# Kernel tuning notes

Hardware: AMD Instinct MI355X
Metric: run time of the kernel (lower is better)

## Reference

```python
import math
import jax, jax.numpy as jnp
import numpy as np

B, S_IN, S_OUT, D_IN, D_OUT = 8, 4096, 1024, 128, 128
EPS = 1e-5


def setup_inputs() -> dict:
    key = jax.random.key(0)
    k0, k1, k2, k3 = jax.random.split(key, 4)
    x = jax.random.normal(k0, (B, S_IN, D_IN), dtype=jnp.float32)
    M = jax.random.uniform(k1, (D_OUT, D_IN), minval=-0.5, maxval=0.5, dtype=jnp.float32)
    P = jax.random.uniform(k2, (D_OUT, D_OUT), minval=-0.1, maxval=0.1, dtype=jnp.float32)
    Linker = jax.random.uniform(k3, (S_IN, S_OUT), minval=-0.1, maxval=0.1, dtype=jnp.float32)
    gamma = jnp.ones((D_OUT,), dtype=jnp.float32)   # LayerNorm weight
    beta = jnp.zeros((D_OUT,), dtype=jnp.float32)   # LayerNorm bias
    return {"x": x, "M": M, "P": P, "Linker": Linker, "gamma": gamma, "beta": beta}


def reference(x, M, P, Linker, gamma, beta):
    # x: (B, S, in_dim) -> out: (B, S_out, out_dim)
    Bsz, S, _ = x.shape
    D = M.shape[0]
    x_trans = x @ M.T                                   # (B, S, D)
    mu = jnp.mean(x_trans, axis=-1, keepdims=True)
    var = jnp.var(x_trans, axis=-1, keepdims=True)      # biased, matches torch LayerNorm
    x_trans = (x_trans - mu) / jnp.sqrt(var + EPS) * gamma + beta
    # periods[i, j] = i*D + j + 2 (registered buffer)
    idx = jnp.arange(D)
    periods = (idx[:, None] * D + idx[None, :] + 2).astype(jnp.float32)  # (D, D)
    k = jnp.arange(S, dtype=jnp.float32)[:, None, None]                   # (S, 1, 1)
    phi = jnp.cos(2.0 * math.pi * k / periods)                            # (S, D, D)
    M_k = P[None, :, :] * phi                                             # (S, D, D)
    Nk = jnp.einsum('bsj,sij->bsi', x_trans, M_k)                         # (B, S, D)
    out = jnp.einsum('bsi,st->bti', Nk, Linker)                           # (B, S_out, D)
    return out
```

## Files before the change

kernel.cpp:

```cpp
#include <hip/hip_runtime.h>
#include <math.h>

#define B_SZ   8
#define S_INN  4096
#define S_OUTT 1024
#define DD     128
#define EPS_LN 1e-5f

typedef _Float16 h2 __attribute__((ext_vector_type(2)));
typedef _Float16 h4 __attribute__((ext_vector_type(4)));
typedef _Float16 h8 __attribute__((ext_vector_type(8)));
typedef float f32x4 __attribute__((ext_vector_type(4)));

#define XN_OFF   0
#define NT_OFF   6291456
#define LT_OFF   8388608

__device__ __forceinline__ void gload16(const void* g, void* l) {
    __builtin_amdgcn_global_load_lds(
        (const __attribute__((address_space(1))) unsigned int*)g,
        (__attribute__((address_space(3))) unsigned int*)l, 16, 0, 0);
}

__device__ __forceinline__ float fdot2_(h2 a, h2 b, float c) {
#if __has_builtin(__builtin_amdgcn_fdot2)
    return __builtin_amdgcn_fdot2(a, b, c, false);
#else
    return fmaf((float)a[0], (float)b[0], fmaf((float)a[1], (float)b[1], c));
#endif
}

__device__ __forceinline__ float fract_(float x) {
#if __has_builtin(__builtin_amdgcn_fractf)
    return __builtin_amdgcn_fractf(x);
#else
    return x - floorf(x);
#endif
}

__global__ __launch_bounds__(256) void kA(const float* __restrict__ x,
                                          const float* __restrict__ M,
                                          const float* __restrict__ gamma,
                                          const float* __restrict__ beta,
                                          _Float16* __restrict__ xn16) {
    __shared__ float Ms[128 * 128];

    const int tid = threadIdx.x;
    #pragma unroll
    for (int k = 0; k < 16; ++k) {
        int e4 = tid + k * 256;
        int i  = e4 >> 5;
        int j4 = e4 & 31;
        float4 v = *(const float4*)&M[i * DD + j4 * 4];
        int igp = (i >> 4) & 7;
        int qp  = (i >> 2) & 3;
        int cp  = i & 3;
        int col = (qp * 8 + igp) * 4 + cp;
        Ms[(j4 * 4 + 0) * 128 + col] = v.x;
        Ms[(j4 * 4 + 1) * 128 + col] = v.y;
        Ms[(j4 * 4 + 2) * 128 + col] = v.z;
        Ms[(j4 * 4 + 3) * 128 + col] = v.w;
    }
    __syncthreads();

    const int ig = tid & 7;
    const int rg = tid >> 3;
    const int row0 = blockIdx.x * 64 + rg * 2;

    float acc[2][16];
    #pragma unroll
    for (int rr = 0; rr < 2; ++rr)
        #pragma unroll
        for (int k = 0; k < 16; ++k) acc[rr][k] = 0.f;

    const float4* xr[2];
    #pragma unroll
    for (int rr = 0; rr < 2; ++rr) xr[rr] = (const float4*)&x[(size_t)(row0 + rr) * DD];

    for (int j4 = 0; j4 < 32; ++j4) {
        float xvf[2][4];
        #pragma unroll
        for (int rr = 0; rr < 2; ++rr) {
            float4 t = xr[rr][j4];
            xvf[rr][0] = t.x; xvf[rr][1] = t.y; xvf[rr][2] = t.z; xvf[rr][3] = t.w;
        }
        #pragma unroll
        for (int c = 0; c < 4; ++c) {
            const float* Mrow = &Ms[(j4 * 4 + c) * 128];
            #pragma unroll
            for (int q = 0; q < 4; ++q) {
                const float4 mv = *(const float4*)&Mrow[(q * 8 + ig) * 4];
                #pragma unroll
                for (int rr = 0; rr < 2; ++rr) {
                    acc[rr][q * 4 + 0] = fmaf(xvf[rr][c], mv.x, acc[rr][q * 4 + 0]);
                    acc[rr][q * 4 + 1] = fmaf(xvf[rr][c], mv.y, acc[rr][q * 4 + 1]);
                    acc[rr][q * 4 + 2] = fmaf(xvf[rr][c], mv.z, acc[rr][q * 4 + 2]);
                    acc[rr][q * 4 + 3] = fmaf(xvf[rr][c], mv.w, acc[rr][q * 4 + 3]);
                }
            }
        }
    }

    float g[16], be[16];
    #pragma unroll
    for (int q = 0; q < 4; ++q) {
        float4 gv = *(const float4*)&gamma[ig * 16 + q * 4];
        float4 bv = *(const float4*)&beta[ig * 16 + q * 4];
        g[q*4+0]=gv.x; g[q*4+1]=gv.y; g[q*4+2]=gv.z; g[q*4+3]=gv.w;
        be[q*4+0]=bv.x; be[q*4+1]=bv.y; be[q*4+2]=bv.z; be[q*4+3]=bv.w;
    }
    #pragma unroll
    for (int rr = 0; rr < 2; ++rr) {
        float s1 = 0.f, s2 = 0.f;
        #pragma unroll
        for (int k = 0; k < 16; ++k) { s1 += acc[rr][k]; s2 = fmaf(acc[rr][k], acc[rr][k], s2); }
        #pragma unroll
        for (int m = 1; m < 8; m <<= 1) {
            s1 += __shfl_xor(s1, m, 64);
            s2 += __shfl_xor(s2, m, 64);
        }
        float mu  = s1 * (1.f / 128.f);
        float var = s2 * (1.f / 128.f) - mu * mu;
        float rstd = rsqrtf(var + EPS_LN);
        _Float16* dst = &xn16[(size_t)(row0 + rr) * DD + ig * 16];
        #pragma unroll
        for (int q = 0; q < 4; ++q) {
            h4 hv;
            hv[0] = (_Float16)((acc[rr][q*4+0] - mu) * rstd * g[q*4+0] + be[q*4+0]);
            hv[1] = (_Float16)((acc[rr][q*4+1] - mu) * rstd * g[q*4+1] + be[q*4+1]);
            hv[2] = (_Float16)((acc[rr][q*4+2] - mu) * rstd * g[q*4+2] + be[q*4+2]);
            hv[3] = (_Float16)((acc[rr][q*4+3] - mu) * rstd * g[q*4+3] + be[q*4+3]);
            *(h4*)&dst[q * 4] = hv;
        }
    }
}

__global__ __launch_bounds__(256) void kB(const _Float16* __restrict__ xn16,
                                          const float* __restrict__ P,
                                          _Float16* __restrict__ NT) {
    const int s0 = blockIdx.x * 8;
    __shared__ _Float16 Ps[128 * 136];
    __shared__ _Float16 xs[8 * 1024];

    const int tid = threadIdx.x;
    #pragma unroll
    for (int k = 0; k < 4; ++k) {
        int c   = tid + k * 256;
        int row = c >> 4;
        int b   = row >> 3, sl = row & 7;
        int kk  = c & 15;
        h8 v = *(const h8*)&xn16[((size_t)b * S_INN + s0 + sl) * DD + kk * 8];
        #pragma unroll
        for (int q = 0; q < 4; ++q) {
            int j2 = kk * 4 + q;
            int slot = (j2 & 15) * 4 + (j2 >> 4);
            *(h2*)&xs[sl * 1024 + slot * 16 + b * 2] = h2{ v[q * 2], v[q * 2 + 1] };
        }
    }
    #pragma unroll
    for (int k = 0; k < 16; ++k) {
        int e4 = tid + k * 256;
        int ip = e4 >> 5, j4 = e4 & 31;
        float4 v = *(const float4*)&P[ip * DD + j4 * 4];
        *(h4*)&Ps[ip * 136 + j4 * 4] = h4{ (_Float16)v.x, (_Float16)v.y,
                                           (_Float16)v.z, (_Float16)v.w };
    }
    __syncthreads();

    const int il = tid >> 2;
    const int jq = tid & 3;
    const int j0base = jq * 32;
    const float s0f = (float)s0;
    const float pb0 = (float)(il * DD + j0base + 2);
    const int bsel = ((jq & 1) << 2) | (jq & 2);

    float invp0[32], invp1[32];
    #pragma unroll
    for (int jj = 0; jj < 32; ++jj) {
        float pf0 = pb0 + (float)jj;
        invp0[jj] = __builtin_amdgcn_rcpf(pf0);
        invp1[jj] = __builtin_amdgcn_rcpf(pf0 + 8192.f);
    }

    h8 st[4];
    #pragma unroll
    for (int s_ = 0; s_ < 4; ++s_) st[s_] = h8{};

    #pragma unroll
    for (int sl = 0; sl < 8; ++sl) {
        const float sf = s0f + (float)sl;
        float acc0[8] = {0,0,0,0,0,0,0,0};
        float acc1[8] = {0,0,0,0,0,0,0,0};

        #pragma unroll
        for (int j8 = 0; j8 < 4; ++j8) {
            h8 p0 = *(const h8*)&Ps[il * 136 + j0base + j8 * 8];
            h8 p1 = *(const h8*)&Ps[(il + 64) * 136 + j0base + j8 * 8];

            h2 w0[4], w1[4];
            #pragma unroll
            for (int cp = 0; cp < 4; ++cp) {
                float wv0[2], wv1[2];
                #pragma unroll
                for (int u = 0; u < 2; ++u) {
                    int c = cp * 2 + u;
                    int jj = j8 * 8 + c;
                    float r0 = fract_(sf * invp0[jj]);
                    wv0[u] = (float)p0[c] * __builtin_amdgcn_cosf(r0);
                    float r1 = fract_(sf * invp1[jj]);
                    wv1[u] = (float)p1[c] * __builtin_amdgcn_cosf(r1);
                }
                w0[cp] = h2{ (_Float16)wv0[0], (_Float16)wv0[1] };
                w1[cp] = h2{ (_Float16)wv1[0], (_Float16)wv1[1] };
            }

            #pragma unroll
            for (int jp = 0; jp < 4; ++jp) {
                int slot = (j8 * 4 + jp) * 4 + jq;
                const h8 xlo = *(const h8*)&xs[sl * 1024 + slot * 16];
                const h8 xhi = *(const h8*)&xs[sl * 1024 + slot * 16 + 8];
                #pragma unroll
                for (int b = 0; b < 4; ++b) {
                    h2 xa = h2{ xlo[b * 2], xlo[b * 2 + 1] };
                    h2 xb = h2{ xhi[b * 2], xhi[b * 2 + 1] };
                    acc0[b]     = fdot2_(w0[jp], xa, acc0[b]);
                    acc0[b + 4] = fdot2_(w0[jp], xb, acc0[b + 4]);
                    acc1[b]     = fdot2_(w1[jp], xa, acc1[b]);
                    acc1[b + 4] = fdot2_(w1[jp], xb, acc1[b + 4]);
                }
            }
        }

        const bool lo1 = (jq & 1) == 0;
        const bool lo2 = (jq & 2) == 0;
        float n0[4], n1[4];
        #pragma unroll
        for (int k = 0; k < 4; ++k) {
            float mine   = lo1 ? acc0[k] : acc0[k + 4];
            float theirs = lo1 ? acc0[k + 4] : acc0[k];
            n0[k] = mine + __shfl_xor(theirs, 1, 64);
            float mine1   = lo1 ? acc1[k] : acc1[k + 4];
            float theirs1 = lo1 ? acc1[k + 4] : acc1[k];
            n1[k] = mine1 + __shfl_xor(theirs1, 1, 64);
        }
        #pragma unroll
        for (int k = 0; k < 2; ++k) {
            float mine   = lo2 ? n0[k] : n0[k + 2];
            float theirs = lo2 ? n0[k + 2] : n0[k];
            float r0 = mine + __shfl_xor(theirs, 2, 64);
            float mine1   = lo2 ? n1[k] : n1[k + 2];
            float theirs1 = lo2 ? n1[k + 2] : n1[k];
            float r1 = mine1 + __shfl_xor(theirs1, 2, 64);
            st[k][sl]     = (_Float16)r0;
            st[2 + k][sl] = (_Float16)r1;
        }
    }

    #pragma unroll
    for (int k = 0; k < 2; ++k) {
        *(h8*)&NT[((size_t)(bsel + k) * DD + il) * S_INN + s0]        = st[k];
        *(h8*)&NT[((size_t)(bsel + k) * DD + il + 64) * S_INN + s0]   = st[2 + k];
    }
}

__global__ __launch_bounds__(256) void kXf(const float* __restrict__ src,
                                           _Float16* __restrict__ dst,
                                           int R, int C) {
    const size_t sb = (size_t)blockIdx.z * (size_t)R * C;
    const int r0 = blockIdx.x * 64, c0 = blockIdx.y * 64;
    __shared__ float tile[64][67];
    const int tid = threadIdx.x;
    {
        const int lr = tid >> 2, lc = (tid & 3) * 16;
        const float4* srow = (const float4*)&src[sb + (size_t)(r0 + lr) * C + c0 + lc];
        float4 v0 = srow[0], v1 = srow[1], v2 = srow[2], v3 = srow[3];
        *(float4*)&tile[lr][lc +  0] = v0;
        *(float4*)&tile[lr][lc +  4] = v1;
        *(float4*)&tile[lr][lc +  8] = v2;
        *(float4*)&tile[lr][lc + 12] = v3;
    }
    __syncthreads();
    {
        const int wc = tid >> 2, wsx = (tid & 3) * 16;
        h8 o0, o1;
        #pragma unroll
        for (int k = 0; k < 8; ++k) o0[k] = (_Float16)tile[wsx + k][wc];
        #pragma unroll
        for (int k = 0; k < 8; ++k) o1[k] = (_Float16)tile[wsx + 8 + k][wc];
        _Float16* drow = &dst[sb + (size_t)(c0 + wc) * R + r0 + wsx];
        *(h8*)&drow[0] = o0;
        *(h8*)&drow[8] = o1;
    }
}

__global__ __launch_bounds__(512) void kC(const _Float16* __restrict__ NT,
                                          const _Float16* __restrict__ LT,
                                          float* __restrict__ part) {
    __shared__ _Float16 lds_pool[4 * 8192];

    const int tid  = threadIdx.x;
    const int lane = tid & 63;
    const int w    = tid >> 6;
    const int wm   = w >> 2;
    const int wn   = w & 3;
    const int lr   = lane & 15;
    const int lh   = lane >> 4;

    const int mt = blockIdx.x >> 3;
    const int nt = blockIdx.x & 7;
    const int kz = blockIdx.y;
    const int t0 = mt * 128;
    const int n0 = nt * 128;
    const int sbase = kz * 1024;

    const int swz = (lr & 7) << 4;

    f32x4 acc[4][2];
    #pragma unroll
    for (int m = 0; m < 4; ++m)
        #pragma unroll
        for (int n = 0; n < 2; ++n) acc[m][n] = (f32x4){0.f, 0.f, 0.f, 0.f};

    auto stage = [&](int buf, int s0) {
        _Float16* base = &lds_pool[buf * 16384];
        #pragma unroll
        for (int ro = 0; ro < 2; ++ro) {
            int idx = tid + ro * 512;
            int r   = idx >> 3;
            int kb  = idx & 7;
            int skb = kb ^ (r & 7);
            gload16(&LT[(size_t)(t0 + r) * S_INN + s0 + skb * 8], base + idx * 8);
            gload16(&NT[(size_t)(n0 + r) * S_INN + s0 + skb * 8], base + 8192 + idx * 8);
        }
    };

    auto compute = [&](int buf) {
        const char* ldsA = (const char*)&lds_pool[buf * 16384];
        const char* ldsB = ldsA + 16384;
        #pragma unroll
        for (int kk = 0; kk < 2; ++kk) {
            const int kb = (kk * 64 + lh * 16) ^ swz;
            h8 a[4], bf[2];
            #pragma unroll
            for (int m = 0; m < 4; ++m)
                a[m] = *(const h8*)(ldsA + (wm * 64 + m * 16 + lr) * 128 + kb);
            #pragma unroll
            for (int n = 0; n < 2; ++n)
                bf[n] = *(const h8*)(ldsB + (wn * 32 + n * 16 + lr) * 128 + kb);
            #pragma unroll
            for (int m = 0; m < 4; ++m)
                #pragma unroll
                for (int n = 0; n < 2; ++n)
                    acc[m][n] = __builtin_amdgcn_mfma_f32_16x16x32_f16(a[m], bf[n], acc[m][n], 0, 0, 0);
        }
    };

    stage(0, sbase);
    __syncthreads();
    for (int st = 0; st < 16; ++st) {
        const int cur = st & 1;
        if (st < 15) stage(cur ^ 1, sbase + (st + 1) * 64);
        compute(cur);
        __syncthreads();
    }

    float* dst = &part[(size_t)(kz * B_SZ + nt) * S_OUTT * DD];
    #pragma unroll
    for (int m = 0; m < 4; ++m) {
        const int t = t0 + wm * 64 + m * 16 + lh * 4;
        #pragma unroll
        for (int n = 0; n < 2; ++n) {
            const int i = wn * 32 + n * 16 + lr;
            #pragma unroll
            for (int r = 0; r < 4; ++r)
                dst[(size_t)(t + r) * DD + i] = acc[m][n][r];
        }
    }
}

__global__ __launch_bounds__(256) void kD(const float* __restrict__ part,
                                          float* __restrict__ out) {
    const int e4 = blockIdx.x * 256 + threadIdx.x;
    const float4* p = (const float4*)part;
    float4 a  = p[e4];
    float4 b1 = p[e4 + 262144];
    float4 c1 = p[e4 + 2 * 262144];
    float4 d1 = p[e4 + 3 * 262144];
    float4 o;
    o.x = a.x + b1.x + c1.x + d1.x;
    o.y = a.y + b1.y + c1.y + d1.y;
    o.z = a.z + b1.z + c1.z + d1.z;
    o.w = a.w + b1.w + c1.w + d1.w;
    ((float4*)out)[e4] = o;
}

extern "C" void kernel_launch(void* const* d_in, const int* in_sizes, int n_in,
                              void* d_out, int out_size, void* d_ws, size_t ws_size,
                              hipStream_t stream) {
    const float* x     = (const float*)d_in[0];
    const float* M     = (const float*)d_in[1];
    const float* P     = (const float*)d_in[2];
    const float* Lk    = (const float*)d_in[3];
    const float* gamma = (const float*)d_in[4];
    const float* beta  = (const float*)d_in[5];
    float* out = (float*)d_out;

    float* wsf = (float*)d_ws;
    _Float16*  xn16 = (_Float16*)(wsf + XN_OFF);
    _Float16*  NT   = (_Float16*)(wsf + NT_OFF);
    _Float16*  LT   = (_Float16*)(wsf + LT_OFF);
    float*     part = wsf + XN_OFF;

    hipLaunchKernelGGL(kA,  dim3(512),        dim3(256), 0, stream, x, M, gamma, beta, xn16);
    hipLaunchKernelGGL(kB,  dim3(512),        dim3(256), 0, stream, xn16, P, NT);
    hipLaunchKernelGGL(kXf, dim3(64, 16, 1),  dim3(256), 0, stream, Lk, LT, S_INN, S_OUTT);
    hipLaunchKernelGGL(kC,  dim3(64, 4),      dim3(512), 0, stream, NT, LT, part);
    hipLaunchKernelGGL(kD,  dim3(1024),       dim3(256), 0, stream, part, out);
}
```

Before: 162.2 us.

## Use MFMA fp16 for input projection GEMM and hoist P loads in kB

Rewrites kA to convert x and M to fp16 in a swizzled LDS layout and compute x@M.T with 16x16x32 f16 MFMA instructions, 128 rows per block. LayerNorm statistics are then reduced across the MFMA output lanes. The grid shrinks to 256 blocks. Separately, kB loads its P row fragments into registers once, before the sl loop, instead of re-reading LDS every iteration. Together these cut FP32 FMA work and LDS traffic, at the cost of fp16 rounding of inputs, narrower 2-byte output stores and higher register pressure in kB.

After: 142.3 us. 1.14x faster.

```diff
diff --git a/kernel.cpp b/kernel.cpp
--- a/kernel.cpp
+++ b/kernel.cpp
@@ -43,94 +43,88 @@
                                           const float* __restrict__ gamma,
                                           const float* __restrict__ beta,
                                           _Float16* __restrict__ xn16) {
-    __shared__ float Ms[128 * 128];
-
-    const int tid = threadIdx.x;
-    #pragma unroll
-    for (int k = 0; k < 16; ++k) {
-        int e4 = tid + k * 256;
-        int i  = e4 >> 5;
-        int j4 = e4 & 31;
-        float4 v = *(const float4*)&M[i * DD + j4 * 4];
-        int igp = (i >> 4) & 7;
-        int qp  = (i >> 2) & 3;
-        int cp  = i & 3;
-        int col = (qp * 8 + igp) * 4 + cp;
-        Ms[(j4 * 4 + 0) * 128 + col] = v.x;
-        Ms[(j4 * 4 + 1) * 128 + col] = v.y;
-        Ms[(j4 * 4 + 2) * 128 + col] = v.z;
-        Ms[(j4 * 4 + 3) * 128 + col] = v.w;
+    __shared__ _Float16 Xs[128 * 128];
+    __shared__ _Float16 Msw[128 * 128];
+
+    const int tid  = threadIdx.x;
+    const int row0 = blockIdx.x * 128;
+
+    {
+        const int rw = tid >> 1, hf = tid & 1;
+        const float4* xsrc = (const float4*)&x[(size_t)(row0 + rw) * DD + hf * 64];
+        const float4* msrc = (const float4*)&M[rw * DD + hf * 64];
+        #pragma unroll
+        for (int q = 0; q < 8; ++q) {
+            float4 v0 = xsrc[q * 2], v1 = xsrc[q * 2 + 1];
+            h8 hx = { (_Float16)v0.x, (_Float16)v0.y, (_Float16)v0.z, (_Float16)v0.w,
+                      (_Float16)v1.x, (_Float16)v1.y, (_Float16)v1.z, (_Float16)v1.w };
+            float4 m0 = msrc[q * 2], m1 = msrc[q * 2 + 1];
+            h8 hm = { (_Float16)m0.x, (_Float16)m0.y, (_Float16)m0.z, (_Float16)m0.w,
+                      (_Float16)m1.x, (_Float16)m1.y, (_Float16)m1.z, (_Float16)m1.w };
+            int c  = hf * 8 + q;
+            int cs = c ^ (rw & 7);
+            *(h8*)&Xs[rw * 128 + cs * 8]  = hx;
+            *(h8*)&Msw[rw * 128 + cs * 8] = hm;
+        }
     }
     __syncthreads();
 
-    const int ig = tid & 7;
-    const int rg = tid >> 3;
-    const int row0 = blockIdx.x * 64 + rg * 2;
-
-    float acc[2][16];
-    #pragma unroll
-    for (int rr = 0; rr < 2; ++rr)
-        #pragma unroll
-        for (int k = 0; k < 16; ++k) acc[rr][k] = 0.f;
-
-    const float4* xr[2];
-    #pragma unroll
-    for (int rr = 0; rr < 2; ++rr) xr[rr] = (const float4*)&x[(size_t)(row0 + rr) * DD];
-
-    for (int j4 = 0; j4 < 32; ++j4) {
-        float xvf[2][4];
-        #pragma unroll
-        for (int rr = 0; rr < 2; ++rr) {
-            float4 t = xr[rr][j4];
-            xvf[rr][0] = t.x; xvf[rr][1] = t.y; xvf[rr][2] = t.z; xvf[rr][3] = t.w;
-        }
-        #pragma unroll
-        for (int c = 0; c < 4; ++c) {
-            const float* Mrow = &Ms[(j4 * 4 + c) * 128];
-            #pragma unroll
-            for (int q = 0; q < 4; ++q) {
-                const float4 mv = *(const float4*)&Mrow[(q * 8 + ig) * 4];
-                #pragma unroll
-                for (int rr = 0; rr < 2; ++rr) {
-                    acc[rr][q * 4 + 0] = fmaf(xvf[rr][c], mv.x, acc[rr][q * 4 + 0]);
-                    acc[rr][q * 4 + 1] = fmaf(xvf[rr][c], mv.y, acc[rr][q * 4 + 1]);
-                    acc[rr][q * 4 + 2] = fmaf(xvf[rr][c], mv.z, acc[rr][q * 4 + 2]);
-                    acc[rr][q * 4 + 3] = fmaf(xvf[rr][c], mv.w, acc[rr][q * 4 + 3]);
-                }
+    const int lane = tid & 63, w = tid >> 6;
+    const int lr = lane & 15, lh = lane >> 4;
+    const int rw0 = w * 32;
+
+    f32x4 acc[2][8];
+    #pragma unroll
+    for (int m = 0; m < 2; ++m)
+        #pragma unroll
+        for (int n = 0; n < 8; ++n) acc[m][n] = (f32x4){0.f, 0.f, 0.f, 0.f};
+
+    #pragma unroll
+    for (int ks = 0; ks < 4; ++ks) {
+        h8 a[2], bb[8];
+        #pragma unroll
+        for (int m = 0; m < 2; ++m) {
+            int row = rw0 + m * 16 + lr;
+            int cj  = (ks * 4 + lh) ^ (row & 7);
+            a[m] = *(const h8*)&Xs[row * 128 + cj * 8];
+        }
+        #pragma unroll
+        for (int n = 0; n < 8; ++n) {
+            int irow = n * 16 + lr;
+            int cj   = (ks * 4 + lh) ^ (irow & 7);
+            bb[n] = *(const h8*)&Msw[irow * 128 + cj * 8];
+        }
+        #pragma unroll
+        for (int m = 0; m < 2; ++m)
+            #pragma unroll
+            for (int n = 0; n < 8; ++n)
+                acc[m][n] = __builtin_amdgcn_mfma_f32_16x16x32_f16(a[m], bb[n], acc[m][n], 0, 0, 0);
+    }
+
+    float g[8], be[8];
+    #pragma unroll
+    for (int n = 0; n < 8; ++n) { g[n] = gamma[n * 16 + lr]; be[n] = beta[n * 16 + lr]; }
+
+    #pragma unroll
+    for (int m = 0; m < 2; ++m) {
+        #pragma unroll
+        for (int r = 0; r < 4; ++r) {
+            float s1 = 0.f, s2 = 0.f;
+            #pragma unroll
+            for (int n = 0; n < 8; ++n) { float v = acc[m][n][r]; s1 += v; s2 = fmaf(v, v, s2); }
+            #pragma unroll
+            for (int mm = 1; mm < 16; mm <<= 1) {
+                s1 += __shfl_xor(s1, mm, 64);
+                s2 += __shfl_xor(s2, mm, 64);
             }
-        }
-    }
-
-    float g[16], be[16];
-    #pragma unroll
-    for (int q = 0; q < 4; ++q) {
-        float4 gv = *(const float4*)&gamma[ig * 16 + q * 4];
-        float4 bv = *(const float4*)&beta[ig * 16 + q * 4];
-        g[q*4+0]=gv.x; g[q*4+1]=gv.y; g[q*4+2]=gv.z; g[q*4+3]=gv.w;
-        be[q*4+0]=bv.x; be[q*4+1]=bv.y; be[q*4+2]=bv.z; be[q*4+3]=bv.w;
-    }
-    #pragma unroll
-    for (int rr = 0; rr < 2; ++rr) {
-        float s1 = 0.f, s2 = 0.f;
-        #pragma unroll
-        for (int k = 0; k < 16; ++k) { s1 += acc[rr][k]; s2 = fmaf(acc[rr][k], acc[rr][k], s2); }
-        #pragma unroll
-        for (int m = 1; m < 8; m <<= 1) {
-            s1 += __shfl_xor(s1, m, 64);
-            s2 += __shfl_xor(s2, m, 64);
-        }
-        float mu  = s1 * (1.f / 128.f);
-        float var = s2 * (1.f / 128.f) - mu * mu;
-        float rstd = rsqrtf(var + EPS_LN);
-        _Float16* dst = &xn16[(size_t)(row0 + rr) * DD + ig * 16];
-        #pragma unroll
-        for (int q = 0; q < 4; ++q) {
-            h4 hv;
-            hv[0] = (_Float16)((acc[rr][q*4+0] - mu) * rstd * g[q*4+0] + be[q*4+0]);
-            hv[1] = (_Float16)((acc[rr][q*4+1] - mu) * rstd * g[q*4+1] + be[q*4+1]);
-            hv[2] = (_Float16)((acc[rr][q*4+2] - mu) * rstd * g[q*4+2] + be[q*4+2]);
-            hv[3] = (_Float16)((acc[rr][q*4+3] - mu) * rstd * g[q*4+3] + be[q*4+3]);
-            *(h4*)&dst[q * 4] = hv;
+            float mu   = s1 * (1.f / 128.f);
+            float var  = s2 * (1.f / 128.f) - mu * mu;
+            float rstd = rsqrtf(var + EPS_LN);
+            int grow = row0 + rw0 + m * 16 + lh * 4 + r;
+            _Float16* dst = &xn16[(size_t)grow * DD];
+            #pragma unroll
+            for (int n = 0; n < 8; ++n)
+                dst[n * 16 + lr] = (_Float16)((acc[m][n][r] - mu) * rstd * g[n] + be[n]);
         }
     }
 }
@@ -181,6 +175,12 @@
         invp0[jj] = __builtin_amdgcn_rcpf(pf0);
         invp1[jj] = __builtin_amdgcn_rcpf(pf0 + 8192.f);
     }
+    h8 p0r[4], p1r[4];
+    #pragma unroll
+    for (int j8 = 0; j8 < 4; ++j8) {
+        p0r[j8] = *(const h8*)&Ps[il * 136 + j0base + j8 * 8];
+        p1r[j8] = *(const h8*)&Ps[(il + 64) * 136 + j0base + j8 * 8];
+    }
 
     h8 st[4];
     #pragma unroll
@@ -194,9 +194,6 @@
 
         #pragma unroll
         for (int j8 = 0; j8 < 4; ++j8) {
-            h8 p0 = *(const h8*)&Ps[il * 136 + j0base + j8 * 8];
-            h8 p1 = *(const h8*)&Ps[(il + 64) * 136 + j0base + j8 * 8];
-
             h2 w0[4], w1[4];
             #pragma unroll
             for (int cp = 0; cp < 4; ++cp) {
@@ -206,9 +203,9 @@
                     int c = cp * 2 + u;
                     int jj = j8 * 8 + c;
                     float r0 = fract_(sf * invp0[jj]);
-                    wv0[u] = (float)p0[c] * __builtin_amdgcn_cosf(r0);
+                    wv0[u] = (float)p0r[j8][c] * __builtin_amdgcn_cosf(r0);
                     float r1 = fract_(sf * invp1[jj]);
-                    wv1[u] = (float)p1[c] * __builtin_amdgcn_cosf(r1);
+                    wv1[u] = (float)p1r[j8][c] * __builtin_amdgcn_cosf(r1);
                 }
                 w0[cp] = h2{ (_Float16)wv0[0], (_Float16)wv0[1] };
                 w1[cp] = h2{ (_Float16)wv1[0], (_Float16)wv1[1] };
@@ -411,7 +408,7 @@
     _Float16*  LT   = (_Float16*)(wsf + LT_OFF);
     float*     part = wsf + XN_OFF;
 
-    hipLaunchKernelGGL(kA,  dim3(512),        dim3(256), 0, stream, x, M, gamma, beta, xn16);
+    hipLaunchKernelGGL(kA,  dim3(256),        dim3(256), 0, stream, x, M, gamma, beta, xn16);
     hipLaunchKernelGGL(kB,  dim3(512),        dim3(256), 0, stream, xn16, P, NT);
     hipLaunchKernelGGL(kXf, dim3(64, 16, 1),  dim3(256), 0, stream, Lk, LT, S_INN, S_OUTT);
     hipLaunchKernelGGL(kC,  dim3(64, 4),      dim3(512), 0, stream, NT, LT, part);
```
